# Performance work log

Measured on AMD Instinct MI355X. Metric: run time of the kernel, lower is better.

## Reference

```python
import jax, jax.numpy as jnp
import numpy as np

EMB = 256
T = 32          # block_size (hardcoded causal mask length)
HEAD = 128      # total head_size
NH = 8          # n_heads
DH = HEAD // NH # 16 per-head size
B = 4096
EPS = 1e-5


def _ln(x, g, b):
    mu = jnp.mean(x, -1, keepdims=True)
    var = jnp.var(x, -1, keepdims=True)
    return (x - mu) * jax.lax.rsqrt(var + EPS) * g + b


def setup_inputs() -> dict:
    key = jax.random.key(0)
    ks = jax.random.split(key, 12)
    s_in = 1.0 / np.sqrt(EMB)
    s_h = 1.0 / np.sqrt(HEAD)
    s_ff = 1.0 / np.sqrt(4 * EMB)
    return {
        "X": jax.random.normal(ks[0], (B, T, EMB), jnp.float32),
        "ln_g": jnp.ones((EMB,), jnp.float32),
        "ln_b": jnp.zeros((EMB,), jnp.float32),
        # per-head Q/K/V projections packed: [EMB, HEAD] == concat of NH [EMB, DH] heads
        "Wq": jax.random.uniform(ks[1], (EMB, HEAD), jnp.float32, -s_in, s_in),
        "bq": jax.random.uniform(ks[2], (HEAD,), jnp.float32, -s_in, s_in),
        "Wk": jax.random.uniform(ks[3], (EMB, HEAD), jnp.float32, -s_in, s_in),
        "bk": jax.random.uniform(ks[4], (HEAD,), jnp.float32, -s_in, s_in),
        "Wv": jax.random.uniform(ks[5], (EMB, HEAD), jnp.float32, -s_in, s_in),
        "bv": jax.random.uniform(ks[6], (HEAD,), jnp.float32, -s_in, s_in),
        "Wo": jax.random.uniform(ks[7], (HEAD, EMB), jnp.float32, -s_h, s_h),
        "bo": jax.random.uniform(ks[8], (EMB,), jnp.float32, -s_h, s_h),
        "W1": jax.random.uniform(ks[9], (EMB, 4 * EMB), jnp.float32, -s_in, s_in),
        "b1": jax.random.uniform(ks[10], (4 * EMB,), jnp.float32, -s_in, s_in),
        "W2": jax.random.uniform(ks[11], (4 * EMB, EMB), jnp.float32, -s_ff, s_ff),
        "b2": jax.random.uniform(jax.random.fold_in(key, 99), (EMB,), jnp.float32, -s_ff, s_ff),
    }


def reference(X, ln_g, ln_b, Wq, bq, Wk, bk, Wv, bv, Wo, bo, W1, b1, W2, b2):
    h = _ln(X, ln_g, ln_b)                              # [B,T,E]
    # packed QKV, split into heads: [B,T,NH,DH]
    Q = (h @ Wq + bq).reshape(B, T, NH, DH)
    K = (h @ Wk + bk).reshape(B, T, NH, DH)
    V = (h @ Wv + bv).reshape(B, T, NH, DH)
    scores = jnp.einsum("bqhd,bkhd->bhqk", Q, K)        # [B,NH,T,T]
    mask = jnp.tril(jnp.ones((T, T), bool))
    # original: masked_fill(-inf) then divide by sqrt(dh); -inf unchanged
    scores = jnp.where(mask, scores / np.sqrt(DH), -jnp.inf)
    attn = jax.nn.softmax(scores, -1)
    ctx = jnp.einsum("bhqk,bkhd->bqhd", attn, V).reshape(B, T, HEAD)
    X = ctx @ Wo + bo + X                               # residual 1
    h2 = _ln(X, ln_g, ln_b)                             # shared LN params
    out = jax.nn.relu(h2 @ W1 + b1) @ W2 + b2 + X       # residual 2
    return out
```

## Files before the change

kernel.cpp:

```cpp
#include <hip/hip_runtime.h>
#include <math.h>

typedef __attribute__((ext_vector_type(8))) __bf16 bf16x8;
typedef __attribute__((ext_vector_type(8))) unsigned short u16x8;
typedef __attribute__((ext_vector_type(4))) unsigned short u16x4;
typedef __attribute__((ext_vector_type(4))) float f32x4;

namespace {
constexpr int EMB = 256;
constexpr int HD  = 128;
constexpr int FF  = 1024;
constexpr float EPSV = 1e-5f;

constexpr int WS_QKV = 0;
constexpr int WS_O   = 98304;
constexpr int WS_1   = 131072;
constexpr int WS_2   = 393216;

__device__ __forceinline__ unsigned short f32_to_bf16(float f) {
    return __builtin_bit_cast(unsigned short, (__bf16)f);
}
__device__ __forceinline__ float bf16_to_f32(unsigned short h) {
    return __builtin_bit_cast(float, ((unsigned int)h) << 16);
}
__device__ __forceinline__ f32x4 mfma16(u16x8 a, u16x8 b, f32x4 c) {
    return __builtin_amdgcn_mfma_f32_16x16x32_bf16(
        __builtin_bit_cast(bf16x8, a), __builtin_bit_cast(bf16x8, b), c, 0, 0, 0);
}
__device__ __forceinline__ int swzB(int row) { return (row & 7) << 4; }

__device__ __forceinline__ u16x8 ldsA256(const unsigned short* base, int row, int k0) {
    int byte = (row * 256 + k0 * 2) ^ swzB(row);
    return *(const u16x8*)((const char*)base + byte);
}
__device__ __forceinline__ u16x8 ldsA512(const unsigned short* base, int row, int k0) {
    int byte = (row * 512 + k0 * 2) ^ swzB(row);
    return *(const u16x8*)((const char*)base + byte);
}
__device__ __forceinline__ u16x8 ldgF(const unsigned short* base, int frag, int lane) {
    return *(const u16x8*)(base + ((size_t)frag * 64 + lane) * 8);
}
}

__global__ __launch_bounds__(256) void wconv(
    const float* __restrict__ Wq, const float* __restrict__ Wk, const float* __restrict__ Wv,
    const float* __restrict__ Wo, const float* __restrict__ W1, const float* __restrict__ W2,
    unsigned short* __restrict__ ws) {
    int e = blockIdx.x * 256 + threadIdx.x;
    int j, lane, kk, nt, n, k;
    float v;
    if (e < WS_O) {
        int t = e; j = t & 7; lane = (t >> 3) & 63; int r2 = t >> 9;
        kk = r2 & 7; nt = r2 >> 3;
        n = nt * 16 + (lane & 15); k = kk * 32 + (lane >> 4) * 8 + j;
        const float* W = (n < 128) ? Wq : ((n < 256) ? Wk : Wv);
        v = W[k * HD + (n & 127)];
    } else if (e < WS_1) {
        int t = e - WS_O; j = t & 7; lane = (t >> 3) & 63; int r2 = t >> 9;
        kk = r2 & 3; nt = r2 >> 2;
        n = nt * 16 + (lane & 15); k = kk * 32 + (lane >> 4) * 8 + j;
        v = Wo[k * EMB + n];
    } else if (e < WS_2) {
        int t = e - WS_1; j = t & 7; lane = (t >> 3) & 63; int r2 = t >> 9;
        kk = r2 & 7; nt = r2 >> 3;
        n = nt * 16 + (lane & 15); k = kk * 32 + (lane >> 4) * 8 + j;
        v = W1[k * FF + n];
    } else {
        int t = e - WS_2; j = t & 7; lane = (t >> 3) & 63; int r2 = t >> 9;
        kk = r2 & 31; nt = r2 >> 5;
        n = nt * 16 + (lane & 15); k = kk * 32 + (lane >> 4) * 8 + j;
        v = W2[k * EMB + n];
    }
    ws[e] = f32_to_bf16(v);
}

__global__ __launch_bounds__(256, 2) void attn_part(
    const float* __restrict__ X, const float* __restrict__ ln_g, const float* __restrict__ ln_b,
    const float* __restrict__ bq, const float* __restrict__ bk, const float* __restrict__ bv,
    const float* __restrict__ bo, const unsigned short* __restrict__ ws,
    float* __restrict__ x1out) {
    __shared__ __attribute__((aligned(16))) char smem[65536];
    unsigned short* hb = (unsigned short*)smem;
    char* Qf           = smem + 16384;
    char* Kf           = smem + 32768;
    char* Vf           = smem + 49152;

    const unsigned short* WTqkv = ws + WS_QKV;
    const unsigned short* WTo   = ws + WS_O;

    const int tid  = threadIdx.x;
    const int wv   = tid >> 6;
    const int mh   = wv & 1;
    const int nh   = wv >> 1;
    const int lane = tid & 63;
    const int lr   = lane & 15;
    const int lh   = lane >> 4;
    const int row0 = blockIdx.x * 32;
    const f32x4 Z  = {0.f, 0.f, 0.f, 0.f};

    {
        const int r = tid >> 3, sub = tid & 7;
        const float* xr = X + (size_t)(row0 + r) * EMB;
        float4 vv[8];
        float s = 0.f, ss = 0.f;
        #pragma unroll
        for (int j = 0; j < 8; ++j) {
            float4 v = *(const float4*)&xr[sub * 4 + j * 32];
            vv[j] = v;
            s  += (v.x + v.y) + (v.z + v.w);
            ss += (v.x * v.x + v.y * v.y) + (v.z * v.z + v.w * v.w);
        }
        #pragma unroll
        for (int w = 1; w < 8; w <<= 1) { s += __shfl_xor(s, w, 64); ss += __shfl_xor(ss, w, 64); }
        float mu  = s * (1.f / EMB);
        float inv = rsqrtf(fmaxf(ss * (1.f / EMB) - mu * mu, 0.f) + EPSV);
        #pragma unroll
        for (int j = 0; j < 8; ++j) {
            int c = sub * 4 + j * 32;
            float4 v = vv[j];
            float4 g4 = *(const float4*)&ln_g[c];
            float4 b4 = *(const float4*)&ln_b[c];
            u16x4 pk;
            pk[0] = f32_to_bf16((v.x - mu) * inv * g4.x + b4.x);
            pk[1] = f32_to_bf16((v.y - mu) * inv * g4.y + b4.y);
            pk[2] = f32_to_bf16((v.z - mu) * inv * g4.z + b4.z);
            pk[3] = f32_to_bf16((v.w - mu) * inv * g4.w + b4.w);
            *(u16x4*)((char*)hb + ((r * 512 + c * 2) ^ swzB(r))) = pk;
        }
    }
    __syncthreads();

    {
        u16x8 afr[8];
        #pragma unroll
        for (int kk = 0; kk < 8; ++kk)
            afr[kk] = ldsA512(hb, mh * 16 + lr, kk * 32 + lh * 8);
        u16x8 bfrA[8], bfrB[8];
        #pragma unroll
        for (int kk = 0; kk < 8; ++kk) bfrA[kk] = ldgF(WTqkv, (nh * 12) * 8 + kk, lane);
        #pragma unroll 1
        for (int ii = 0; ii < 6; ++ii) {
            int nt0 = nh * 12 + ii * 2;
            #pragma unroll
            for (int kk = 0; kk < 8; ++kk) bfrB[kk] = ldgF(WTqkv, (nt0 + 1) * 8 + kk, lane);
            {
                f32x4 e = Z, o = Z;
                #pragma unroll
                for (int kk = 0; kk < 8; kk += 2) {
                    e = mfma16(afr[kk], bfrA[kk], e);
                    o = mfma16(afr[kk + 1], bfrA[kk + 1], o);
                }
                f32x4 a = e + o;
                int gcol = nt0 * 16 + lr;
                int mat = gcol >> 7, c = gcol & 127;
                const float* bias = (mat == 0) ? bq : ((mat == 1) ? bk : bv);
                float bc = bias[c];
                char* regbase = smem + 16384 + mat * 16384;
                #pragma unroll
                for (int reg = 0; reg < 4; ++reg) {
                    int r0 = mh * 16 + lh * 4 + reg;
                    *(float*)(regbase + ((r0 * 512 + c * 4) ^ swzB(r0))) = a[reg] + bc;
                }
            }
            if (ii < 5) {
                #pragma unroll
                for (int kk = 0; kk < 8; ++kk) bfrA[kk] = ldgF(WTqkv, (nt0 + 2) * 8 + kk, lane);
            }
            {
                f32x4 e = Z, o = Z;
                #pragma unroll
                for (int kk = 0; kk < 8; kk += 2) {
                    e = mfma16(afr[kk], bfrB[kk], e);
                    o = mfma16(afr[kk + 1], bfrB[kk + 1], o);
                }
                f32x4 a = e + o;
                int gcol = (nt0 + 1) * 16 + lr;
                int mat = gcol >> 7, c = gcol & 127;
                const float* bias = (mat == 0) ? bq : ((mat == 1) ? bk : bv);
                float bc = bias[c];
                char* regbase = smem + 16384 + mat * 16384;
                #pragma unroll
                for (int reg = 0; reg < 4; ++reg) {
                    int r0 = mh * 16 + lh * 4 + reg;
                    *(float*)(regbase + ((r0 * 512 + c * 4) ^ swzB(r0))) = a[reg] + bc;
                }
            }
        }
    }
    __syncthreads();

    {
        const int hd = tid >> 5, q = tid & 31;
        float qreg[16];
        #pragma unroll
        for (int t = 0; t < 4; ++t) {
            float4 v = *(const float4*)(Qf + ((q * 512 + hd * 64 + t * 16) ^ swzB(q)));
            qreg[t * 4 + 0] = v.x; qreg[t * 4 + 1] = v.y;
            qreg[t * 4 + 2] = v.z; qreg[t * 4 + 3] = v.w;
        }
        unsigned int ps[16];
        float mmax = -1e30f;
        #pragma unroll
        for (int k = 0; k < 32; ++k) {
            float s_ = 0.f;
            #pragma unroll
            for (int t = 0; t < 4; ++t) {
                float4 v = *(const float4*)(Kf + ((k * 512 + hd * 64 + t * 16) ^ swzB(k)));
                s_ += qreg[t * 4 + 0] * v.x + qreg[t * 4 + 1] * v.y
                    + qreg[t * 4 + 2] * v.z + qreg[t * 4 + 3] * v.w;
            }
            s_ *= 0.25f;
            unsigned short us = f32_to_bf16(s_);
            if ((k & 1) == 0) ps[k >> 1] = (unsigned int)us;
            else              ps[k >> 1] |= ((unsigned int)us) << 16;
            if (k <= q) mmax = fmaxf(mmax, bf16_to_f32(us));
        }
        float den = 0.f;
        float ctx[16];
        #pragma unroll
        for (int j = 0; j < 16; ++j) ctx[j] = 0.f;
        #pragma unroll
        for (int k = 0; k < 32; ++k) {
            unsigned short us = (unsigned short)((k & 1) ? (ps[k >> 1] >> 16) : (ps[k >> 1] & 0xFFFFu));
            float e = (k <= q) ? __expf(bf16_to_f32(us) - mmax) : 0.f;
            den += e;
            #pragma unroll
            for (int t = 0; t < 4; ++t) {
                float4 v = *(const float4*)(Vf + ((k * 512 + hd * 64 + t * 16) ^ swzB(k)));
                ctx[t * 4 + 0] += e * v.x; ctx[t * 4 + 1] += e * v.y;
                ctx[t * 4 + 2] += e * v.z; ctx[t * 4 + 3] += e * v.w;
            }
        }
        float rd = 1.f / den;
        u16x8 o0, o1;
        #pragma unroll
        for (int j = 0; j < 8; ++j) { o0[j] = f32_to_bf16(ctx[j] * rd); o1[j] = f32_to_bf16(ctx[8 + j] * rd); }
        int by0 = (q * 256 + hd * 32) ^ swzB(q);
        int by1 = (q * 256 + hd * 32 + 16) ^ swzB(q);
        *(u16x8*)((char*)hb + by0) = o0;
        *(u16x8*)((char*)hb + by1) = o1;
    }
    __syncthreads();

    {
        u16x8 afr[4];
        #pragma unroll
        for (int kk = 0; kk < 4; ++kk)
            afr[kk] = ldsA256(hb, mh * 16 + lr, kk * 32 + lh * 8);
        u16x8 bfrA[4], bfrB[4];
        #pragma unroll
        for (int kk = 0; kk < 4; ++kk) bfrA[kk] = ldgF(WTo, (nh * 8) * 4 + kk, lane);
        #pragma unroll 1
        for (int ii = 0; ii < 4; ++ii) {
            int nt0 = nh * 8 + ii * 2;
            #pragma unroll
            for (int kk = 0; kk < 4; ++kk) bfrB[kk] = ldgF(WTo, (nt0 + 1) * 4 + kk, lane);
            {
                int col = nt0 * 16 + lr;
                float bc = bo[col];
                f32x4 e = Z, o = Z;
                e = mfma16(afr[0], bfrA[0], e);
                o = mfma16(afr[1], bfrA[1], o);
                e = mfma16(afr[2], bfrA[2], e);
                o = mfma16(afr[3], bfrA[3], o);
                f32x4 a = e + o;
                #pragma unroll
                for (int reg = 0; reg < 4; ++reg) {
                    int r0 = mh * 16 + lh * 4 + reg;
                    size_t gi = (size_t)(row0 + r0) * EMB + col;
                    x1out[gi] = a[reg] + bc + X[gi];
                }
            }
            if (ii < 3) {
                #pragma unroll
                for (int kk = 0; kk < 4; ++kk) bfrA[kk] = ldgF(WTo, (nt0 + 2) * 4 + kk, lane);
            }
            {
                int col = (nt0 + 1) * 16 + lr;
                float bc = bo[col];
                f32x4 e = Z, o = Z;
                e = mfma16(afr[0], bfrB[0], e);
                o = mfma16(afr[1], bfrB[1], o);
                e = mfma16(afr[2], bfrB[2], e);
                o = mfma16(afr[3], bfrB[3], o);
                f32x4 a = e + o;
                #pragma unroll
                for (int reg = 0; reg < 4; ++reg) {
                    int r0 = mh * 16 + lh * 4 + reg;
                    size_t gi = (size_t)(row0 + r0) * EMB + col;
                    x1out[gi] = a[reg] + bc + X[gi];
                }
            }
        }
    }
}

__global__ __launch_bounds__(512, 1) void ffn_part(
    const float* __restrict__ ln_g, const float* __restrict__ ln_b,
    const float* __restrict__ b1, const float* __restrict__ b2,
    const unsigned short* __restrict__ ws, float* __restrict__ io) {
    __shared__ __attribute__((aligned(16))) char smem[49152];
    unsigned short* h2  = (unsigned short*)smem;
    unsigned short* fch = (unsigned short*)(smem + 32768);

    const unsigned short* WT1 = ws + WS_1;
    const unsigned short* WT2 = ws + WS_2;

    const int tid  = threadIdx.x;
    const int wv   = tid >> 6;
    const int lane = tid & 63;
    const int lr   = lane & 15;
    const int lh   = lane >> 4;
    const int row0 = blockIdx.x * 64;
    const f32x4 Z  = {0.f, 0.f, 0.f, 0.f};

    {
        const int r = tid >> 3, sub = tid & 7;
        const float* xr = io + (size_t)(row0 + r) * EMB;
        float4 vv[8];
        float s = 0.f, ss = 0.f;
        #pragma unroll
        for (int j = 0; j < 8; ++j) {
            float4 v = *(const float4*)&xr[sub * 4 + j * 32];
            vv[j] = v;
            s  += (v.x + v.y) + (v.z + v.w);
            ss += (v.x * v.x + v.y * v.y) + (v.z * v.z + v.w * v.w);
        }
        #pragma unroll
        for (int w = 1; w < 8; w <<= 1) { s += __shfl_xor(s, w, 64); ss += __shfl_xor(ss, w, 64); }
        float mu  = s * (1.f / EMB);
        float inv = rsqrtf(fmaxf(ss * (1.f / EMB) - mu * mu, 0.f) + EPSV);
        #pragma unroll
        for (int j = 0; j < 8; ++j) {
            int c = sub * 4 + j * 32;
            float4 v = vv[j];
            float4 g4 = *(const float4*)&ln_g[c];
            float4 b4 = *(const float4*)&ln_b[c];
            u16x4 pk;
            pk[0] = f32_to_bf16((v.x - mu) * inv * g4.x + b4.x);
            pk[1] = f32_to_bf16((v.y - mu) * inv * g4.y + b4.y);
            pk[2] = f32_to_bf16((v.z - mu) * inv * g4.z + b4.z);
            pk[3] = f32_to_bf16((v.w - mu) * inv * g4.w + b4.w);
            *(u16x4*)((char*)h2 + ((r * 512 + c * 2) ^ swzB(r))) = pk;
        }
    }
    __syncthreads();

    {
        f32x4 acc2[4][2];
        #pragma unroll
        for (int mt = 0; mt < 4; ++mt) { acc2[mt][0] = Z; acc2[mt][1] = Z; }

        #pragma unroll 1
        for (int ch = 0; ch < 8; ++ch) {
            {
                int fn = ch * 8 + wv;
                u16x8 bAll[8];
                #pragma unroll
                for (int kk = 0; kk < 8; ++kk) bAll[kk] = ldgF(WT1, fn * 8 + kk, lane);
                float bc = b1[fn * 16 + lr];
                int cc = wv * 16 + lr;
                #pragma unroll 1
                for (int mt = 0; mt < 4; ++mt) {
                    u16x8 afr[8];
                    #pragma unroll
                    for (int kk = 0; kk < 8; ++kk)
                        afr[kk] = ldsA512(h2, mt * 16 + lr, kk * 32 + lh * 8);
                    f32x4 e = Z, o = Z;
                    #pragma unroll
                    for (int kk = 0; kk < 8; kk += 2) {
                        e = mfma16(afr[kk], bAll[kk], e);
                        o = mfma16(afr[kk + 1], bAll[kk + 1], o);
                    }
                    f32x4 a = e + o;
                    #pragma unroll
                    for (int reg = 0; reg < 4; ++reg) {
                        int r0 = mt * 16 + lh * 4 + reg;
                        *(unsigned short*)((char*)fch + ((r0 * 256 + cc * 2) ^ swzB(r0))) =
                            f32_to_bf16(fmaxf(a[reg] + bc, 0.f));
                    }
                }
            }
            __syncthreads();
            #pragma unroll
            for (int i = 0; i < 2; ++i) {
                u16x8 b2f[4];
                #pragma unroll
                for (int kk = 0; kk < 4; ++kk)
                    b2f[kk] = ldgF(WT2, (wv * 2 + i) * 32 + ch * 4 + kk, lane);
                #pragma unroll
                for (int mt = 0; mt < 4; ++mt) {
                    u16x8 afr2[4];
                    #pragma unroll
                    for (int kk = 0; kk < 4; ++kk)
                        afr2[kk] = ldsA256(fch, mt * 16 + lr, kk * 32 + lh * 8);
                    f32x4 t = acc2[mt][i];
                    t = mfma16(afr2[0], b2f[0], t);
                    t = mfma16(afr2[1], b2f[1], t);
                    t = mfma16(afr2[2], b2f[2], t);
                    t = mfma16(afr2[3], b2f[3], t);
                    acc2[mt][i] = t;
                }
            }
            __syncthreads();
        }
        #pragma unroll
        for (int i = 0; i < 2; ++i) {
            int col = (wv * 2 + i) * 16 + lr;
            float bc = b2[col];
            #pragma unroll
            for (int mt = 0; mt < 4; ++mt) {
                #pragma unroll
                for (int reg = 0; reg < 4; ++reg) {
                    int r0 = mt * 16 + lh * 4 + reg;
                    size_t gi = (size_t)(row0 + r0) * EMB + col;
                    io[gi] = acc2[mt][i][reg] + bc + io[gi];
                }
            }
        }
    }
}

extern "C" void kernel_launch(void* const* d_in, const int* in_sizes, int n_in,
                              void* d_out, int out_size, void* d_ws, size_t ws_size,
                              hipStream_t stream) {
    const float* X    = (const float*)d_in[0];
    const float* ln_g = (const float*)d_in[1];
    const float* ln_b = (const float*)d_in[2];
    const float* Wq   = (const float*)d_in[3];
    const float* bq   = (const float*)d_in[4];
    const float* Wk   = (const float*)d_in[5];
    const float* bk   = (const float*)d_in[6];
    const float* Wv   = (const float*)d_in[7];
    const float* bv   = (const float*)d_in[8];
    const float* Wo   = (const float*)d_in[9];
    const float* bo   = (const float*)d_in[10];
    const float* W1   = (const float*)d_in[11];
    const float* b1   = (const float*)d_in[12];
    const float* W2   = (const float*)d_in[13];
    const float* b2   = (const float*)d_in[14];
    unsigned short* ws = (unsigned short*)d_ws;
    float* O = (float*)d_out;

    wconv<<<2560, 256, 0, stream>>>(Wq, Wk, Wv, Wo, W1, W2, ws);
    attn_part<<<4096, 256, 0, stream>>>(X, ln_g, ln_b, bq, bk, bv, bo, ws, O);
    ffn_part<<<2048, 512, 0, stream>>>(ln_g, ln_b, b1, b2, ws, O);
}
```

Before: 348.0 us.

## Fuse attention and FFN kernels into one block kernel keeping residual in LDS

Merges the attention and FFN kernels into a single kernel of 32 rows per 256-thread block. The post-attention residual X1 is kept in shared memory instead of being written to and re-read from global memory. The FFN loop is re-tiled for 4 waves over 32 rows, so each block streams W1/W2 for half as many rows as before and per-row weight traffic roughly doubles. LDS regions are reused across phases, which requires correct synchronisation.

```diff
diff --git a/kernel.cpp b/kernel.cpp
--- a/kernel.cpp
+++ b/kernel.cpp
@@ -74,19 +74,23 @@
     ws[e] = f32_to_bf16(v);
 }
 
-__global__ __launch_bounds__(256, 2) void attn_part(
+__global__ __launch_bounds__(256, 2) void fused_block(
     const float* __restrict__ X, const float* __restrict__ ln_g, const float* __restrict__ ln_b,
     const float* __restrict__ bq, const float* __restrict__ bk, const float* __restrict__ bv,
-    const float* __restrict__ bo, const unsigned short* __restrict__ ws,
-    float* __restrict__ x1out) {
+    const float* __restrict__ bo, const float* __restrict__ b1, const float* __restrict__ b2,
+    const unsigned short* __restrict__ ws, float* __restrict__ out) {
     __shared__ __attribute__((aligned(16))) char smem[65536];
     unsigned short* hb = (unsigned short*)smem;
-    char* Qf           = smem + 16384;
-    char* Kf           = smem + 32768;
-    char* Vf           = smem + 49152;
+    char* Qf  = smem + 16384;
+    char* Kf  = smem + 32768;
+    char* Vf  = smem + 49152;
+    char* X1f = smem + 16384;
+    unsigned short* fch = (unsigned short*)(smem + 49152);
 
     const unsigned short* WTqkv = ws + WS_QKV;
     const unsigned short* WTo   = ws + WS_O;
+    const unsigned short* WT1   = ws + WS_1;
+    const unsigned short* WT2   = ws + WS_2;
 
     const int tid  = threadIdx.x;
     const int wv   = tid >> 6;
@@ -247,81 +251,38 @@
         #pragma unroll
         for (int kk = 0; kk < 4; ++kk)
             afr[kk] = ldsA256(hb, mh * 16 + lr, kk * 32 + lh * 8);
-        u16x8 bfrA[4], bfrB[4];
-        #pragma unroll
-        for (int kk = 0; kk < 4; ++kk) bfrA[kk] = ldgF(WTo, (nh * 8) * 4 + kk, lane);
         #pragma unroll 1
-        for (int ii = 0; ii < 4; ++ii) {
-            int nt0 = nh * 8 + ii * 2;
-            #pragma unroll
-            for (int kk = 0; kk < 4; ++kk) bfrB[kk] = ldgF(WTo, (nt0 + 1) * 4 + kk, lane);
-            {
-                int col = nt0 * 16 + lr;
-                float bc = bo[col];
-                f32x4 e = Z, o = Z;
-                e = mfma16(afr[0], bfrA[0], e);
-                o = mfma16(afr[1], bfrA[1], o);
-                e = mfma16(afr[2], bfrA[2], e);
-                o = mfma16(afr[3], bfrA[3], o);
-                f32x4 a = e + o;
-                #pragma unroll
-                for (int reg = 0; reg < 4; ++reg) {
-                    int r0 = mh * 16 + lh * 4 + reg;
-                    size_t gi = (size_t)(row0 + r0) * EMB + col;
-                    x1out[gi] = a[reg] + bc + X[gi];
-                }
-            }
-            if (ii < 3) {
-                #pragma unroll
-                for (int kk = 0; kk < 4; ++kk) bfrA[kk] = ldgF(WTo, (nt0 + 2) * 4 + kk, lane);
-            }
-            {
-                int col = (nt0 + 1) * 16 + lr;
-                float bc = bo[col];
-                f32x4 e = Z, o = Z;
-                e = mfma16(afr[0], bfrB[0], e);
-                o = mfma16(afr[1], bfrB[1], o);
-                e = mfma16(afr[2], bfrB[2], e);
-                o = mfma16(afr[3], bfrB[3], o);
-                f32x4 a = e + o;
-                #pragma unroll
-                for (int reg = 0; reg < 4; ++reg) {
-                    int r0 = mh * 16 + lh * 4 + reg;
-                    size_t gi = (size_t)(row0 + r0) * EMB + col;
-                    x1out[gi] = a[reg] + bc + X[gi];
-                }
-            }
-        }
-    }
-}
-
-__global__ __launch_bounds__(512, 1) void ffn_part(
-    const float* __restrict__ ln_g, const float* __restrict__ ln_b,
-    const float* __restrict__ b1, const float* __restrict__ b2,
-    const unsigned short* __restrict__ ws, float* __restrict__ io) {
-    __shared__ __attribute__((aligned(16))) char smem[49152];
-    unsigned short* h2  = (unsigned short*)smem;
-    unsigned short* fch = (unsigned short*)(smem + 32768);
-
-    const unsigned short* WT1 = ws + WS_1;
-    const unsigned short* WT2 = ws + WS_2;
-
-    const int tid  = threadIdx.x;
-    const int wv   = tid >> 6;
-    const int lane = tid & 63;
-    const int lr   = lane & 15;
-    const int lh   = lane >> 4;
-    const int row0 = blockIdx.x * 64;
-    const f32x4 Z  = {0.f, 0.f, 0.f, 0.f};
+        for (int i = 0; i < 8; ++i) {
+            int nt = nh * 8 + i;
+            u16x8 bfr[4];
+            #pragma unroll
+            for (int kk = 0; kk < 4; ++kk) bfr[kk] = ldgF(WTo, nt * 4 + kk, lane);
+            int col = nt * 16 + lr;
+            float bc = bo[col];
+            f32x4 e = Z, o = Z;
+            e = mfma16(afr[0], bfr[0], e);
+            o = mfma16(afr[1], bfr[1], o);
+            e = mfma16(afr[2], bfr[2], e);
+            o = mfma16(afr[3], bfr[3], o);
+            f32x4 a = e + o;
+            #pragma unroll
+            for (int reg = 0; reg < 4; ++reg) {
+                int r0 = mh * 16 + lh * 4 + reg;
+                float xv = X[(size_t)(row0 + r0) * EMB + col];
+                *(float*)(X1f + ((r0 * 1024 + col * 4) ^ swzB(r0))) = a[reg] + bc + xv;
+            }
+        }
+    }
+    __syncthreads();
 
     {
         const int r = tid >> 3, sub = tid & 7;
-        const float* xr = io + (size_t)(row0 + r) * EMB;
         float4 vv[8];
         float s = 0.f, ss = 0.f;
         #pragma unroll
         for (int j = 0; j < 8; ++j) {
-            float4 v = *(const float4*)&xr[sub * 4 + j * 32];
+            int c = sub * 4 + j * 32;
+            float4 v = *(const float4*)(X1f + ((r * 1024 + c * 4) ^ swzB(r)));
             vv[j] = v;
             s  += (v.x + v.y) + (v.z + v.w);
             ss += (v.x * v.x + v.y * v.y) + (v.z * v.z + v.w * v.w);
@@ -341,31 +302,34 @@
             pk[1] = f32_to_bf16((v.y - mu) * inv * g4.y + b4.y);
             pk[2] = f32_to_bf16((v.z - mu) * inv * g4.z + b4.z);
             pk[3] = f32_to_bf16((v.w - mu) * inv * g4.w + b4.w);
-            *(u16x4*)((char*)h2 + ((r * 512 + c * 2) ^ swzB(r))) = pk;
+            *(u16x4*)((char*)hb + ((r * 512 + c * 2) ^ swzB(r))) = pk;
         }
     }
     __syncthreads();
 
     {
-        f32x4 acc2[4][2];
-        #pragma unroll
-        for (int mt = 0; mt < 4; ++mt) { acc2[mt][0] = Z; acc2[mt][1] = Z; }
+        f32x4 acc2[2][4];
+        #pragma unroll
+        for (int mt = 0; mt < 2; ++mt)
+            #pragma unroll
+            for (int i = 0; i < 4; ++i) acc2[mt][i] = Z;
 
         #pragma unroll 1
         for (int ch = 0; ch < 8; ++ch) {
-            {
-                int fn = ch * 8 + wv;
+            #pragma unroll
+            for (int f = 0; f < 2; ++f) {
+                int fn = ch * 8 + wv * 2 + f;
                 u16x8 bAll[8];
                 #pragma unroll
                 for (int kk = 0; kk < 8; ++kk) bAll[kk] = ldgF(WT1, fn * 8 + kk, lane);
                 float bc = b1[fn * 16 + lr];
-                int cc = wv * 16 + lr;
+                int cc = (wv * 2 + f) * 16 + lr;
                 #pragma unroll 1
-                for (int mt = 0; mt < 4; ++mt) {
+                for (int mt = 0; mt < 2; ++mt) {
                     u16x8 afr[8];
                     #pragma unroll
                     for (int kk = 0; kk < 8; ++kk)
-                        afr[kk] = ldsA512(h2, mt * 16 + lr, kk * 32 + lh * 8);
+                        afr[kk] = ldsA512(hb, mt * 16 + lr, kk * 32 + lh * 8);
                     f32x4 e = Z, o = Z;
                     #pragma unroll
                     for (int kk = 0; kk < 8; kk += 2) {
@@ -382,39 +346,47 @@
                 }
             }
             __syncthreads();
-            #pragma unroll
-            for (int i = 0; i < 2; ++i) {
-                u16x8 b2f[4];
-                #pragma unroll
-                for (int kk = 0; kk < 4; ++kk)
-                    b2f[kk] = ldgF(WT2, (wv * 2 + i) * 32 + ch * 4 + kk, lane);
-                #pragma unroll
-                for (int mt = 0; mt < 4; ++mt) {
-                    u16x8 afr2[4];
+            {
+                u16x8 afr2[2][4];
+                #pragma unroll
+                for (int mt = 0; mt < 2; ++mt)
                     #pragma unroll
                     for (int kk = 0; kk < 4; ++kk)
-                        afr2[kk] = ldsA256(fch, mt * 16 + lr, kk * 32 + lh * 8);
-                    f32x4 t = acc2[mt][i];
-                    t = mfma16(afr2[0], b2f[0], t);
-                    t = mfma16(afr2[1], b2f[1], t);
-                    t = mfma16(afr2[2], b2f[2], t);
-                    t = mfma16(afr2[3], b2f[3], t);
-                    acc2[mt][i] = t;
+                        afr2[mt][kk] = ldsA256(fch, mt * 16 + lr, kk * 32 + lh * 8);
+                #pragma unroll 1
+                for (int i = 0; i < 4; ++i) {
+                    u16x8 b2f[4];
+                    #pragma unroll
+                    for (int kk = 0; kk < 4; ++kk)
+                        b2f[kk] = ldgF(WT2, (wv * 4 + i) * 32 + ch * 4 + kk, lane);
+                    f32x4 t0 = acc2[0][i];
+                    t0 = mfma16(afr2[0][0], b2f[0], t0);
+                    t0 = mfma16(afr2[0][1], b2f[1], t0);
+                    t0 = mfma16(afr2[0][2], b2f[2], t0);
+                    t0 = mfma16(afr2[0][3], b2f[3], t0);
+                    acc2[0][i] = t0;
+                    f32x4 t1 = acc2[1][i];
+                    t1 = mfma16(afr2[1][0], b2f[0], t1);
+                    t1 = mfma16(afr2[1][1], b2f[1], t1);
+                    t1 = mfma16(afr2[1][2], b2f[2], t1);
+                    t1 = mfma16(afr2[1][3], b2f[3], t1);
+                    acc2[1][i] = t1;
                 }
             }
             __syncthreads();
         }
-        #pragma unroll
-        for (int i = 0; i < 2; ++i) {
-            int col = (wv * 2 + i) * 16 + lr;
+        float* outp = out + (size_t)row0 * EMB;
+        #pragma unroll
+        for (int i = 0; i < 4; ++i) {
+            int col = (wv * 4 + i) * 16 + lr;
             float bc = b2[col];
             #pragma unroll
-            for (int mt = 0; mt < 4; ++mt) {
+            for (int mt = 0; mt < 2; ++mt) {
                 #pragma unroll
                 for (int reg = 0; reg < 4; ++reg) {
                     int r0 = mt * 16 + lh * 4 + reg;
-                    size_t gi = (size_t)(row0 + r0) * EMB + col;
-                    io[gi] = acc2[mt][i][reg] + bc + io[gi];
+                    float x1 = *(const float*)(X1f + ((r0 * 1024 + col * 4) ^ swzB(r0)));
+                    outp[(size_t)r0 * EMB + col] = acc2[mt][i][reg] + bc + x1;
                 }
             }
         }
@@ -443,6 +415,5 @@
     float* O = (float*)d_out;
 
     wconv<<<2560, 256, 0, stream>>>(Wq, Wk, Wv, Wo, W1, W2, ws);
-    attn_part<<<4096, 256, 0, stream>>>(X, ln_g, ln_b, bq, bk, bv, bo, ws, O);
-    ffn_part<<<2048, 512, 0, stream>>>(ln_g, ln_b, b1, b2, ws, O);
-}
+    fused_block<<<4096, 256, 0, stream>>>(X, ln_g, ln_b, bq, bk, bv, bo, b1, b2, ws, O);
+}
```

After: 381.9 us. 1.1x slower.
